# Optimization experiments

Hardware: AMD Instinct MI355X
Metric: run time of the kernel (lower is better)

## Reference

```python
import jax, jax.numpy as jnp
import numpy as np

T, S, F, A, P = 64, 32, 256, 64, 32  # t, s, feature_len, attn_len, posembed_len


def setup_inputs() -> dict:
    key = jax.random.key(0)
    ks = jax.random.split(key, 8)
    w = lambda k, shape: jax.random.normal(k, shape, dtype=jnp.float32) * 0.02
    return {
        "batch_data": jax.random.normal(ks[0], (T * S, F), dtype=jnp.float32),
        "positions": jax.random.normal(ks[1], (2, S, S, 9), dtype=jnp.float32),
        "temp": jax.random.normal(ks[2], (T, T, S, 10), dtype=jnp.float32),
        "Wa": w(ks[3], (F, A)), "ba": jnp.zeros((A,), jnp.float32),
        "Wb": w(ks[4], (F + 2 * P, A)), "bb": jnp.zeros((A,), jnp.float32),
        "Wg": w(ks[5], (F + 2 * P, F)), "bg": jnp.zeros((F,), jnp.float32),
        "Wpos": w(ks[6], (9, P)), "bpos": jnp.zeros((P,), jnp.float32),
        "Wtmp": w(ks[7], (10, 2 * P)), "btmp": jnp.zeros((2 * P,), jnp.float32),
    }


def reference(batch_data, positions, temp, Wa, ba, Wb, bb, Wg, bg, Wpos, bpos, Wtmp, btmp):
    x = batch_data.reshape(T, S, F)                      # (T,S,F)
    # pairwise spatial embedding: pos[j,k] used for query node j, key node k
    pos = jnp.concatenate([positions[0] @ Wpos + bpos,
                           positions[1] @ Wpos + bpos], axis=-1)  # (S,S,2P)
    tmp = temp @ Wtmp + btmp                              # (T,T,S,2P)
    theta = x @ Wa + ba                                   # (T,S,A)

    # Linear on concat([x, p]) == x @ W[:F] + p @ W[F:] + b; split to avoid
    # materializing the broadcast concatenated tensor.
    WbX, WbP = Wb[:F], Wb[F:]
    WgX, WgP = Wg[:F], Wg[F:]
    x_phi = x @ WbX                                       # (T,S,A)
    x_g = x @ WgX                                         # (T,S,F)

    # ---- spatial pass: keys over nodes k at same time ----
    phi_s = x_phi[None] + (pos @ WbP)[:, None] + bb       # (Sq,T,Sk,A)
    feat_s = x_g[None] + (pos @ WgP)[:, None] + bg        # (Sq,T,Sk,F)
    scores_s = jnp.einsum('ija,jika->ijk', theta, phi_s)  # (T,Sq,Sk)
    attn_s = jax.nn.softmax(scores_s, axis=-1)
    res = jnp.einsum('ijk,jikf->ijf', attn_s, feat_s)     # (T,S,F)

    # ---- temporal pass: keys over times tau at same node ----
    phi_t = x_phi[None] + tmp @ WbP + bb                  # (Tq,T,S,A)
    feat_t = x_g[None] + tmp @ WgP + bg                   # (Tq,T,S,F)
    scores_t = jnp.einsum('jia,jtia->jit', theta, phi_t)  # (Tq,S,Tk)
    attn_t = jax.nn.softmax(scores_t, axis=-1)
    res = res + jnp.einsum('jit,jtif->jif', attn_t, feat_t)
    return res                                            # (T,S,F)
```

## Files before the change

kernel.cpp:

```cpp
#include <hip/hip_runtime.h>
#include <hip/hip_fp16.h>

constexpr int T = 64, S = 32, F = 256, A = 64;
constexpr int R = T * S;

constexpr size_t OFF_XPH = 0;
constexpr size_t OFF_TH  = OFF_XPH + (size_t)R * A;
constexpr size_t OFF_UU  = OFF_TH  + (size_t)R * A;
constexpr size_t OFF_DD  = OFF_UU  + (size_t)R * A;
constexpr size_t OFF_POS = OFF_DD  + (size_t)R * 16;
constexpr size_t OFF_XGH = OFF_POS + (size_t)S * S * 64;

constexpr int XLS = 68;

__device__ __forceinline__ float dot4(float4 a, float4 b) {
    return a.x * b.x + a.y * b.y + a.z * b.z + a.w * b.w;
}
__device__ __forceinline__ float4 f4fma(float s, float4 v, float4 a) {
    a.x += s * v.x; a.y += s * v.y; a.z += s * v.z; a.w += s * v.w; return a;
}
__device__ __forceinline__ float4 f4add(float4 a, float4 b) {
    a.x += b.x; a.y += b.y; a.z += b.z; a.w += b.w; return a;
}
__device__ __forceinline__ float4 ldh4(const __half* p, size_t idx4) {
    float2 raw = ((const float2*)p)[idx4];
    const __half2* h = reinterpret_cast<const __half2*>(&raw);
    const float2 lo = __half22float2(h[0]);
    const float2 hi = __half22float2(h[1]);
    return make_float4(lo.x, lo.y, hi.x, hi.y);
}

__global__ __launch_bounds__(256) void k_pre(
    const float* __restrict__ bd, const float* __restrict__ Wa,
    const float* __restrict__ ba, const float* __restrict__ Wb,
    const float* __restrict__ Wg, const float* __restrict__ Wtmp,
    const float* __restrict__ positions, const float* __restrict__ Wpos,
    const float* __restrict__ bpos,
    float* __restrict__ xph, float* __restrict__ th,
    float* __restrict__ uu, float* __restrict__ dd,
    float* __restrict__ pos, __half* __restrict__ XG_h)
{
    const int blk = blockIdx.x;
    const int tid = threadIdx.x;

    __shared__ float xs[8 * 256];
    __shared__ float ths[8][64];
    __shared__ float us[8][64];

    if (blk >= 256) {
        const int xb = blk - 256;
        {
            const int idx = xb * 256 + tid;
            const int p = idx & 63, jk = idx >> 6;
            const int e = p >> 5, pp = p & 31;
            const float* src = positions + (size_t)(e * 1024 + jk) * 9;
            float acc = bpos[pp];
#pragma unroll
            for (int q = 0; q < 9; ++q) acc += src[q] * Wpos[q * 32 + pp];
            pos[idx] = acc;
        }
        {
            const float4* src = (const float4*)(bd + (size_t)xb * 8 * 256);
            float4* dst = (float4*)xs;
            dst[tid] = src[tid];
            dst[tid + 256] = src[tid + 256];
        }
        __syncthreads();
        float acc[8] = {0.f, 0.f, 0.f, 0.f, 0.f, 0.f, 0.f, 0.f};
#pragma unroll
        for (int c0 = 0; c0 < 256; c0 += 8) {
            float wv[8];
#pragma unroll
            for (int j = 0; j < 8; ++j) wv[j] = Wg[(size_t)(c0 + j) * 256 + tid];
#pragma unroll
            for (int j = 0; j < 8; ++j) {
#pragma unroll
                for (int r = 0; r < 8; ++r) acc[r] += xs[r * 256 + c0 + j] * wv[j];
            }
        }
#pragma unroll
        for (int r = 0; r < 8; ++r)
            XG_h[(size_t)(xb * 8 + r) * 256 + tid] = __float2half(acc[r]);
        return;
    }

    const int w = tid >> 6, lane = tid & 63;
    const int row0 = blk * 8 + 2 * w;

    {
        const float4* src = (const float4*)(bd + (size_t)blk * 8 * 256);
        float4* dst = (float4*)xs;
        dst[tid] = src[tid];
        dst[tid + 256] = src[tid + 256];
    }
    __syncthreads();

    const float* x0 = xs + (2 * w) * 256;
    const float* x1 = xs + (2 * w + 1) * 256;
    float accA0 = ba[lane], accA1 = accA0, accB0 = 0.f, accB1 = 0.f;
#pragma unroll
    for (int c0 = 0; c0 < 256; c0 += 8) {
        float wa[8], wb[8];
#pragma unroll
        for (int j = 0; j < 8; ++j) wa[j] = Wa[(c0 + j) * 64 + lane];
#pragma unroll
        for (int j = 0; j < 8; ++j) wb[j] = Wb[(c0 + j) * 64 + lane];
#pragma unroll
        for (int j = 0; j < 8; ++j) {
            const float xa = x0[c0 + j], xb2 = x1[c0 + j];
            accA0 += xa * wa[j]; accA1 += xb2 * wa[j];
            accB0 += xa * wb[j]; accB1 += xb2 * wb[j];
        }
    }
    th[(size_t)row0 * 64 + lane] = accA0;
    th[(size_t)(row0 + 1) * 64 + lane] = accA1;
    xph[(size_t)row0 * 64 + lane] = accB0;
    xph[(size_t)(row0 + 1) * 64 + lane] = accB1;
    ths[2 * w][lane] = accA0; ths[2 * w + 1][lane] = accA1;
    __syncthreads();

    float accU0 = 0.f, accU1 = 0.f;
#pragma unroll 8
    for (int a = 0; a < 64; ++a) {
        const float wp = Wb[(256 + lane) * 64 + a];
        accU0 += ths[2 * w][a] * wp;
        accU1 += ths[2 * w + 1][a] * wp;
    }
    uu[(size_t)row0 * 64 + lane] = accU0;
    uu[(size_t)(row0 + 1) * 64 + lane] = accU1;
    us[2 * w][lane] = accU0; us[2 * w + 1][lane] = accU1;
    __syncthreads();

    const int rsel = lane >> 4, q = lane & 15;
    if (rsel < 2 && q < 10) {
        float accD = 0.f;
#pragma unroll 8
        for (int p2 = 0; p2 < 64; ++p2) accD += us[2 * w + rsel][p2] * Wtmp[q * 64 + p2];
        dd[(size_t)(row0 + rsel) * 16 + q] = accD;
    }
}

__global__ __launch_bounds__(256) void k_fuse(
    const float* __restrict__ temp, const float* __restrict__ Wtmp,
    const float* __restrict__ btmp, const float* __restrict__ Wg,
    const float* __restrict__ bg, const float* __restrict__ xph,
    const float* __restrict__ th, const float* __restrict__ uu,
    const float* __restrict__ dd, const float* __restrict__ pos,
    const __half* __restrict__ XG_h, float* __restrict__ out)
{
    const int ss = blockIdx.x >> 4;
    const int tt0 = (blockIdx.x & 15) * 4;
    const int tid = threadIdx.x;
    const int w = tid >> 6, lane = tid & 63;

    __shared__ float th_s[4][64], u_s[4][64], d_s[4][16];
    __shared__ float es[4][32], et[4][64], w10[4][10];
    __shared__ float gs[4][64];
    __shared__ float xphL[64 * XLS];
    __shared__ float4 zz4[4][64];
    __shared__ float4 part4[4][4][64];
    __shared__ float4 part4b[4][4][64];

    {
        const size_t r = (size_t)(tt0 + w) * 32 + ss;
        th_s[w][lane] = th[r * 64 + lane];
        u_s[w][lane]  = uu[r * 64 + lane];
        if (lane < 16) d_s[w][lane] = dd[r * 16 + lane];
    }
    for (int i = tid; i < 64 * 64; i += 256) {
        const int row = i >> 6, a = i & 63;
        xphL[row * XLS + a] = xph[((size_t)row * 32 + ss) * 64 + a];
    }
    __syncthreads();

    {
        const int t = lane;
        const float4* xp = (const float4*)&xphL[t * XLS];
        const float4* tv4 = (const float4*)th_s[w];
        float sc = 0.f;
#pragma unroll
        for (int a = 0; a < 16; ++a) sc += dot4(xp[a], tv4[a]);
        const float2* tp = (const float2*)(temp + (((size_t)(tt0 + w) * 64 + t) * 32 + ss) * 10);
        const float2* dv = (const float2*)d_s[w];
        float2 tmpv[5];
#pragma unroll
        for (int q = 0; q < 5; ++q) {
            tmpv[q] = tp[q];
            const float2 d2 = dv[q];
            sc += tmpv[q].x * d2.x + tmpv[q].y * d2.y;
        }
        float m = sc;
#pragma unroll
        for (int off = 32; off; off >>= 1) m = fmaxf(m, __shfl_xor(m, off));
        const float e = __expf(sc - m);
        float s = e;
#pragma unroll
        for (int off = 32; off; off >>= 1) s += __shfl_xor(s, off);
        const float at = e / s;
        et[w][t] = at;
        float r10[10];
#pragma unroll
        for (int q = 0; q < 5; ++q) { r10[2 * q] = at * tmpv[q].x; r10[2 * q + 1] = at * tmpv[q].y; }
#pragma unroll
        for (int off = 32; off; off >>= 1) {
#pragma unroll
            for (int i = 0; i < 10; ++i) r10[i] += __shfl_xor(r10[i], off);
        }
        if (lane == 0) {
#pragma unroll
            for (int i = 0; i < 10; ++i) w10[w][i] = r10[i];
        }
    }

    if (tid < 128) {
        const int ttl = tid >> 5, k = tid & 31;
        const float4* xp = (const float4*)(xph + ((size_t)(tt0 + ttl) * 32 + k) * 64);
        const float4* pp = (const float4*)(pos + ((size_t)ss * 32 + k) * 64);
        const float4* tv4 = (const float4*)th_s[ttl];
        const float4* uv4 = (const float4*)u_s[ttl];
        float sc = 0.f;
#pragma unroll
        for (int a = 0; a < 16; ++a) sc += dot4(xp[a], tv4[a]) + dot4(pp[a], uv4[a]);
        float m = sc;
#pragma unroll
        for (int off = 16; off; off >>= 1) m = fmaxf(m, __shfl_xor(m, off));
        const float e = __expf(sc - m);
        float s = e;
#pragma unroll
        for (int off = 16; off; off >>= 1) s += __shfl_xor(s, off);
        es[ttl][k] = e / s;
    }
    __syncthreads();

    {
        const int p = lane;
        const float* pb = pos + (size_t)ss * 32 * 64 + p;
        float pv = 0.f;
#pragma unroll
        for (int k0 = 0; k0 < 32; k0 += 8) {
            float yv[8];
#pragma unroll
            for (int j = 0; j < 8; ++j) yv[j] = pb[(size_t)(k0 + j) * 64];
#pragma unroll
            for (int j = 0; j < 8; ++j) pv += es[w][k0 + j] * yv[j];
        }
        float g = pv + btmp[p];
#pragma unroll
        for (int q = 0; q < 10; ++q) g += w10[w][q] * Wtmp[q * 64 + p];
        gs[w][p] = g;
    }

    {
        float4 acc[4];
#pragma unroll
        for (int r = 0; r < 4; ++r) acc[r] = make_float4(0.f, 0.f, 0.f, 0.f);
#pragma unroll
        for (int j = 0; j < 16; ++j) {
            const int t = 16 * w + j;
            const float4 x4 = ldh4(XG_h, ((size_t)t * 32 + ss) * 64 + lane);
#pragma unroll
            for (int r = 0; r < 4; ++r) acc[r] = f4fma(et[r][t], x4, acc[r]);
        }
#pragma unroll
        for (int r = 0; r < 4; ++r) part4[w][r][lane] = acc[r];
    }
    __syncthreads();

    {
        float4 a = make_float4(0.f, 0.f, 0.f, 0.f);
#pragma unroll
        for (int k = 0; k < 32; ++k) {
            const float4 x4 = ldh4(XG_h, ((size_t)(tt0 + w) * 32 + k) * 64 + lane);
            a = f4fma(es[w][k], x4, a);
        }
#pragma unroll
        for (int w2 = 0; w2 < 4; ++w2) a = f4add(a, part4[w2][w][lane]);
        zz4[w][lane] = a;
    }
    {
        const float4* Wg4 = (const float4*)Wg;
        float4 acc[4];
#pragma unroll
        for (int r = 0; r < 4; ++r) acc[r] = make_float4(0.f, 0.f, 0.f, 0.f);
#pragma unroll
        for (int j = 0; j < 16; ++j) {
            const int pp = 16 * w + j;
            const float4 wg = Wg4[(size_t)(256 + pp) * 64 + lane];
#pragma unroll
            for (int r = 0; r < 4; ++r) acc[r] = f4fma(gs[r][pp], wg, acc[r]);
        }
#pragma unroll
        for (int r = 0; r < 4; ++r) part4b[w][r][lane] = acc[r];
    }
    __syncthreads();

    {
        float4 o = f4add(zz4[w][lane], part4b[0][w][lane]);
        o = f4add(o, part4b[1][w][lane]);
        o = f4add(o, part4b[2][w][lane]);
        o = f4add(o, part4b[3][w][lane]);
        const float4 b4 = ((const float4*)bg)[lane];
        o.x += 2.f * b4.x; o.y += 2.f * b4.y; o.z += 2.f * b4.z; o.w += 2.f * b4.w;
        ((float4*)out)[((size_t)(tt0 + w) * 32 + ss) * 64 + lane] = o;
    }
}

extern "C" void kernel_launch(void* const* d_in, const int* in_sizes, int n_in,
                              void* d_out, int out_size, void* d_ws, size_t ws_size,
                              hipStream_t stream) {
    const float* bd   = (const float*)d_in[0];
    const float* positions = (const float*)d_in[1];
    const float* temp = (const float*)d_in[2];
    const float* Wa   = (const float*)d_in[3];
    const float* ba   = (const float*)d_in[4];
    const float* Wb   = (const float*)d_in[5];
    const float* Wg   = (const float*)d_in[7];
    const float* bg   = (const float*)d_in[8];
    const float* Wpos = (const float*)d_in[9];
    const float* bpos = (const float*)d_in[10];
    const float* Wtmp = (const float*)d_in[11];
    const float* btmp = (const float*)d_in[12];
    float* out = (float*)d_out;

    float* ws  = (float*)d_ws;
    float* xph = ws + OFF_XPH;
    float* th  = ws + OFF_TH;
    float* uu  = ws + OFF_UU;
    float* dd  = ws + OFF_DD;
    float* pos = ws + OFF_POS;
    __half* XG_h = (__half*)(ws + OFF_XGH);

    k_pre<<<512, 256, 0, stream>>>(bd, Wa, ba, Wb, Wg, Wtmp, positions, Wpos,
                                   bpos, xph, th, uu, dd, pos, XG_h);
    k_fuse<<<512, 256, 0, stream>>>(temp, Wtmp, btmp, Wg, bg,
                                    xph, th, uu, dd, pos, XG_h, out);
}
```

Baseline: 111.3 us.

## Split fuse kernel into two-timestep blocks with hoisted XG loads and rebalanced warps

Each k_fuse block now covers 2 query timesteps instead of 4, doubling the grid to 1024 blocks. The block index mapping now puts the node index in the low bits. Warps 0-1 compute the temporal softmax while warps 2-3 compute the spatial scores, splitting each dot product across half-waves. The XG half-precision loads are issued into registers early, the xph tile is loaded as float4, and launch bounds request 4 blocks per CU. The aim is more parallelism and latency hiding. The cost is that the per-block xph tile load and the Wg weight reads are now repeated twice as often.

```diff
diff --git a/kernel.cpp b/kernel.cpp
--- a/kernel.cpp
+++ b/kernel.cpp
@@ -22,8 +22,7 @@
 __device__ __forceinline__ float4 f4add(float4 a, float4 b) {
     a.x += b.x; a.y += b.y; a.z += b.z; a.w += b.w; return a;
 }
-__device__ __forceinline__ float4 ldh4(const __half* p, size_t idx4) {
-    float2 raw = ((const float2*)p)[idx4];
+__device__ __forceinline__ float4 h4tof4(float2 raw) {
     const __half2* h = reinterpret_cast<const __half2*>(&raw);
     const float2 lo = __half22float2(h[0]);
     const float2 hi = __half22float2(h[1]);
@@ -140,7 +139,7 @@
     }
 }
 
-__global__ __launch_bounds__(256) void k_fuse(
+__global__ __launch_bounds__(256, 4) void k_fuse(
     const float* __restrict__ temp, const float* __restrict__ Wtmp,
     const float* __restrict__ btmp, const float* __restrict__ Wg,
     const float* __restrict__ bg, const float* __restrict__ xph,
@@ -148,32 +147,35 @@
     const float* __restrict__ dd, const float* __restrict__ pos,
     const __half* __restrict__ XG_h, float* __restrict__ out)
 {
-    const int ss = blockIdx.x >> 4;
-    const int tt0 = (blockIdx.x & 15) * 4;
+    const int ss = blockIdx.x & 31;
+    const int tt0 = (blockIdx.x >> 5) * 2;
     const int tid = threadIdx.x;
     const int w = tid >> 6, lane = tid & 63;
 
-    __shared__ float th_s[4][64], u_s[4][64], d_s[4][16];
-    __shared__ float es[4][32], et[4][64], w10[4][10];
-    __shared__ float gs[4][64];
     __shared__ float xphL[64 * XLS];
-    __shared__ float4 zz4[4][64];
-    __shared__ float4 part4[4][4][64];
-    __shared__ float4 part4b[4][4][64];
-
-    {
+    __shared__ float th_s[2][64], u_s[2][64], d_s[2][16];
+    __shared__ float es[2][32], et[2][64], w10[2][10];
+    __shared__ float gs[2][64];
+    __shared__ float4 zzp[4][64];
+    __shared__ float4 part4[4][2][64];
+    __shared__ float4 part4b[4][2][64];
+
+    if (w < 2) {
         const size_t r = (size_t)(tt0 + w) * 32 + ss;
         th_s[w][lane] = th[r * 64 + lane];
         u_s[w][lane]  = uu[r * 64 + lane];
         if (lane < 16) d_s[w][lane] = dd[r * 16 + lane];
     }
-    for (int i = tid; i < 64 * 64; i += 256) {
-        const int row = i >> 6, a = i & 63;
-        xphL[row * XLS + a] = xph[((size_t)row * 32 + ss) * 64 + a];
-    }
-    __syncthreads();
-
-    {
+#pragma unroll
+    for (int k2 = 0; k2 < 4; ++k2) {
+        const int i = tid + 256 * k2;
+        const int row = i >> 4, c = i & 15;
+        const float4 v = ((const float4*)xph)[((size_t)row * 32 + ss) * 16 + c];
+        *(float4*)&xphL[row * XLS + 4 * c] = v;
+    }
+    __syncthreads();
+
+    if (w < 2) {
         const int t = lane;
         const float4* xp = (const float4*)&xphL[t * XLS];
         const float4* tv4 = (const float4*)th_s[w];
@@ -210,17 +212,17 @@
 #pragma unroll
             for (int i = 0; i < 10; ++i) w10[w][i] = r10[i];
         }
-    }
-
-    if (tid < 128) {
-        const int ttl = tid >> 5, k = tid & 31;
-        const float4* xp = (const float4*)(xph + ((size_t)(tt0 + ttl) * 32 + k) * 64);
-        const float4* pp = (const float4*)(pos + ((size_t)ss * 32 + k) * 64);
-        const float4* tv4 = (const float4*)th_s[ttl];
-        const float4* uv4 = (const float4*)u_s[ttl];
+    } else {
+        const int r = w - 2;
+        const int k = lane & 31, half = lane >> 5;
+        const float4* key = half
+            ? (const float4*)(pos + ((size_t)ss * 32 + k) * 64)
+            : (const float4*)(xph + ((size_t)(tt0 + r) * 32 + k) * 64);
+        const float4* qv = half ? (const float4*)u_s[r] : (const float4*)th_s[r];
         float sc = 0.f;
 #pragma unroll
-        for (int a = 0; a < 16; ++a) sc += dot4(xp[a], tv4[a]) + dot4(pp[a], uv4[a]);
+        for (int a = 0; a < 16; ++a) sc += dot4(key[a], qv[a]);
+        sc += __shfl_xor(sc, 32);
         float m = sc;
 #pragma unroll
         for (int off = 16; off; off >>= 1) m = fmaxf(m, __shfl_xor(m, off));
@@ -228,11 +230,17 @@
         float s = e;
 #pragma unroll
         for (int off = 16; off; off >>= 1) s += __shfl_xor(s, off);
-        es[ttl][k] = e / s;
-    }
-    __syncthreads();
-
-    {
+        if (half == 0) es[r][k] = e / s;
+    }
+    __syncthreads();
+
+    float2 rawT[16];
+#pragma unroll
+    for (int j = 0; j < 16; ++j) {
+        const int t = 16 * w + j;
+        rawT[j] = ((const float2*)XG_h)[((size_t)t * 32 + ss) * 64 + lane];
+    }
+    if (w < 2) {
         const int p = lane;
         const float* pb = pos + (size_t)ss * 32 * 64 + p;
         float pv = 0.f;
@@ -249,56 +257,53 @@
         for (int q = 0; q < 10; ++q) g += w10[w][q] * Wtmp[q * 64 + p];
         gs[w][p] = g;
     }
-
     {
-        float4 acc[4];
-#pragma unroll
-        for (int r = 0; r < 4; ++r) acc[r] = make_float4(0.f, 0.f, 0.f, 0.f);
+        float4 a0 = make_float4(0.f, 0.f, 0.f, 0.f), a1 = a0;
 #pragma unroll
         for (int j = 0; j < 16; ++j) {
             const int t = 16 * w + j;
-            const float4 x4 = ldh4(XG_h, ((size_t)t * 32 + ss) * 64 + lane);
-#pragma unroll
-            for (int r = 0; r < 4; ++r) acc[r] = f4fma(et[r][t], x4, acc[r]);
-        }
-#pragma unroll
-        for (int r = 0; r < 4; ++r) part4[w][r][lane] = acc[r];
+            const float4 x4 = h4tof4(rawT[j]);
+            a0 = f4fma(et[0][t], x4, a0);
+            a1 = f4fma(et[1][t], x4, a1);
+        }
+        part4[w][0][lane] = a0;
+        part4[w][1][lane] = a1;
     }
     __syncthreads();
 
     {
+        const int r = w & 1, kh = (w >> 1) * 16;
+        float2 rawS[16];
+#pragma unroll
+        for (int j = 0; j < 16; ++j)
+            rawS[j] = ((const float2*)XG_h)[((size_t)(tt0 + r) * 32 + kh + j) * 64 + lane];
         float4 a = make_float4(0.f, 0.f, 0.f, 0.f);
 #pragma unroll
-        for (int k = 0; k < 32; ++k) {
-            const float4 x4 = ldh4(XG_h, ((size_t)(tt0 + w) * 32 + k) * 64 + lane);
-            a = f4fma(es[w][k], x4, a);
-        }
-#pragma unroll
-        for (int w2 = 0; w2 < 4; ++w2) a = f4add(a, part4[w2][w][lane]);
-        zz4[w][lane] = a;
+        for (int j = 0; j < 16; ++j)
+            a = f4fma(es[r][kh + j], h4tof4(rawS[j]), a);
+        zzp[w][lane] = a;
     }
     {
         const float4* Wg4 = (const float4*)Wg;
-        float4 acc[4];
-#pragma unroll
-        for (int r = 0; r < 4; ++r) acc[r] = make_float4(0.f, 0.f, 0.f, 0.f);
+        float4 b0 = make_float4(0.f, 0.f, 0.f, 0.f), b1 = b0;
 #pragma unroll
         for (int j = 0; j < 16; ++j) {
             const int pp = 16 * w + j;
             const float4 wg = Wg4[(size_t)(256 + pp) * 64 + lane];
-#pragma unroll
-            for (int r = 0; r < 4; ++r) acc[r] = f4fma(gs[r][pp], wg, acc[r]);
-        }
-#pragma unroll
-        for (int r = 0; r < 4; ++r) part4b[w][r][lane] = acc[r];
-    }
-    __syncthreads();
-
-    {
-        float4 o = f4add(zz4[w][lane], part4b[0][w][lane]);
-        o = f4add(o, part4b[1][w][lane]);
-        o = f4add(o, part4b[2][w][lane]);
-        o = f4add(o, part4b[3][w][lane]);
+            b0 = f4fma(gs[0][pp], wg, b0);
+            b1 = f4fma(gs[1][pp], wg, b1);
+        }
+        part4b[w][0][lane] = b0;
+        part4b[w][1][lane] = b1;
+    }
+    __syncthreads();
+
+    if (w < 2) {
+        float4 o = f4add(zzp[w][lane], zzp[2 + w][lane]);
+#pragma unroll
+        for (int w2 = 0; w2 < 4; ++w2) o = f4add(o, part4[w2][w][lane]);
+#pragma unroll
+        for (int w2 = 0; w2 < 4; ++w2) o = f4add(o, part4b[w2][w][lane]);
         const float4 b4 = ((const float4*)bg)[lane];
         o.x += 2.f * b4.x; o.y += 2.f * b4.y; o.z += 2.f * b4.z; o.w += 2.f * b4.w;
         ((float4*)out)[((size_t)(tt0 + w) * 32 + ss) * 64 + lane] = o;
@@ -332,6 +337,6 @@
 
     k_pre<<<512, 256, 0, stream>>>(bd, Wa, ba, Wb, Wg, Wtmp, positions, Wpos,
                                    bpos, xph, th, uu, dd, pos, XG_h);
-    k_fuse<<<512, 256, 0, stream>>>(temp, Wtmp, btmp, Wg, bg,
-                                    xph, th, uu, dd, pos, XG_h, out);
-}
+    k_fuse<<<1024, 256, 0, stream>>>(temp, Wtmp, btmp, Wg, bg,
+                                     xph, th, uu, dd, pos, XG_h, out);
+}
```

After: 111.4 us. Within noise of the previous version (+0.1%).
